# Performance work log

Measured on AMD Instinct MI355X. Metric: run time of the kernel, lower is better.

Reference implementation:

```python
import jax, jax.numpy as jnp
import numpy as np

ZETA = 1.03
GAMMA = -0.03


def setup_inputs() -> dict:
    key = jax.random.key(0)
    k1, k2, k3 = jax.random.split(key, 3)
    B, S, H, D = 2, 2048, 16, 128
    return {
        "query_states": jax.random.normal(k1, (B * S, H, D), dtype=jnp.float32),
        "key_states": jax.random.normal(k2, (B * S, H, D), dtype=jnp.float32),
        "value_states": jax.random.normal(k3, (B * S, H, D), dtype=jnp.float32),
        "batch_size": B,
        "q_length": S,
        "kv_length": S,
    }


def reference(query_states, key_states, value_states, batch_size, q_length, kv_length):
    H = query_states.shape[1]
    D = query_states.shape[2]
    # [B*S, H, D] -> [B, S, H, D]
    q = query_states.reshape(batch_size, q_length, H, D)
    k = key_states.reshape(batch_size, kv_length, H, D)
    v = value_states.reshape(batch_size, kv_length, H, D)
    # scores: [B, H, Q, K]
    scores = jnp.einsum("bqhd,bkhd->bhqk", q, k) / jnp.sqrt(jnp.float32(D)).astype(q.dtype)
    causal = jnp.triu(jnp.ones((q_length, kv_length), dtype=bool), k=1)  # True above diagonal
    scores = jnp.where(causal[None, None, :, :], -jnp.inf, scores)
    probs = jax.nn.softmax(scores, axis=-1)
    # clipped softmax (fp8 recipe): clip((zeta-gamma)*p + gamma, 0, 1)
    probs = jnp.clip((ZETA - GAMMA) * probs + GAMMA, 0.0, 1.0)
    out = jnp.einsum("bhqk,bkhd->bqhd", probs, v)
    return out.reshape(batch_size * q_length, H, D)
```

## Files before the change

### kernel.cpp

```cpp
#include <hip/hip_runtime.h>

typedef __attribute__((ext_vector_type(4))) float f32x4;
typedef __attribute__((ext_vector_type(8))) short bf16x8;
typedef __attribute__((ext_vector_type(4))) int   i32x4;
typedef __attribute__((ext_vector_type(2))) int   i32x2;

#define B_ 2
#define S_ 2048
#define H_ 16
#define D_ 128
#define RS_ (H_ * D_)
#define LOG2E 1.44269504088896340736f
#define ZG 1.06f
#define GM (-0.03f)
#define QSC (0.08838834764831845f * LOG2E)

__device__ __forceinline__ ushort f2bf(float x) {
    uint u = __builtin_bit_cast(uint, x);
    u += 0x7FFFu + ((u >> 16) & 1u);
    return (ushort)(u >> 16);
}

__device__ __forceinline__ void gld16(const void* g, void* l) {
    __builtin_amdgcn_global_load_lds(
        (const __attribute__((address_space(1))) unsigned int*)g,
        (__attribute__((address_space(3))) unsigned int*)l, 16, 0, 0);
}

__global__ __launch_bounds__(256)
void prep_kv(const float* __restrict__ Kg, const float* __restrict__ Vg,
             ushort* __restrict__ Kb, ushort* __restrict__ Vt)
{
    __shared__ ushort Vl[64 * 136];
    const int t = threadIdx.x;
    if (blockIdx.x < 512) {
        const int n  = blockIdx.x;
        const int bh = n >> 4;
        const int ch = n & 15;
        const int s  = ch * 128 + (t >> 1);
        const int d0 = (t & 1) * 64;
        const int b  = bh >> 4, h = bh & 15;
        const float* in = Kg + (((size_t)b * S_ + s) * H_ + h) * D_ + d0;
        ushort* out = Kb + ((size_t)bh * S_ + s) * D_ + d0;
#pragma unroll
        for (int j = 0; j < 4; ++j) {
            f32x4 x0 = *(const f32x4*)(in + j * 16);
            f32x4 x1 = *(const f32x4*)(in + j * 16 + 4);
            f32x4 x2 = *(const f32x4*)(in + j * 16 + 8);
            f32x4 x3 = *(const f32x4*)(in + j * 16 + 12);
            union { ushort u[16]; i32x4 v[2]; } p;
#pragma unroll
            for (int i = 0; i < 4; ++i) {
                p.u[i]      = f2bf(x0[i]);
                p.u[4 + i]  = f2bf(x1[i]);
                p.u[8 + i]  = f2bf(x2[i]);
                p.u[12 + i] = f2bf(x3[i]);
            }
            *(i32x4*)(out + j * 16)     = p.v[0];
            *(i32x4*)(out + j * 16 + 8) = p.v[1];
        }
    } else {
        const int n  = blockIdx.x - 512;
        const int bh = n >> 5;
        const int kt = n & 31;
        const int b  = bh >> 4, h = bh & 15;
#pragma unroll
        for (int it = 0; it < 2; ++it) {
            const int r  = it * 32 + (t >> 3);
            const int c0 = (t & 7) * 16;
            const int s  = kt * 64 + r;
            const float* in = Vg + (((size_t)b * S_ + s) * H_ + h) * D_ + c0;
            f32x4 x0 = *(const f32x4*)(in);
            f32x4 x1 = *(const f32x4*)(in + 4);
            f32x4 x2 = *(const f32x4*)(in + 8);
            f32x4 x3 = *(const f32x4*)(in + 12);
            union { ushort u[16]; i32x4 v[2]; } p;
#pragma unroll
            for (int i = 0; i < 4; ++i) {
                p.u[i]      = f2bf(x0[i]);
                p.u[4 + i]  = f2bf(x1[i]);
                p.u[8 + i]  = f2bf(x2[i]);
                p.u[12 + i] = f2bf(x3[i]);
            }
            *(i32x4*)(Vl + r * 136 + c0)     = p.v[0];
            *(i32x4*)(Vl + r * 136 + c0 + 8) = p.v[1];
        }
        __syncthreads();
        const int d  = t >> 1;
        const int kh = (t & 1) * 32;
        ushort* out = Vt + ((size_t)bh * 32 + kt) * 8192 + d * 64 + kh;
        uint wds[16];
#pragma unroll
        for (int i = 0; i < 16; ++i) {
            uint a = Vl[(kh + 2 * i) * 136 + d];
            uint c = Vl[(kh + 2 * i + 1) * 136 + d];
            wds[i] = a | (c << 16);
        }
#pragma unroll
        for (int j = 0; j < 4; ++j)
            *(i32x4*)(out + j * 8) = *(i32x4*)&wds[j * 4];
    }
}

__global__ __launch_bounds__(256, 3)
void attn_one(const float* __restrict__ Qg, const ushort* __restrict__ Kb,
              const ushort* __restrict__ Vt, float* __restrict__ Og)
{
    __shared__ char SHc[32768 + 4 * 2304];

    const int tid  = threadIdx.x;
    const int w    = tid >> 6;
    const int lane = tid & 63;
    const int g    = lane >> 4;
    const int l15  = lane & 15;
    char* const Kl = SHc;
    char* const Vl = SHc + 16384;
    char* const pB = SHc + 32768 + w * 2304;

    const int n  = blockIdx.x;
    const int qt = 31 - (n >> 5);
    const int bh = n & 31;
    const int b  = bh >> 4, h = bh & 15;

    const int q0  = qt * 64;
    const int qw0 = q0 + w * 16;
    const int qme = qw0 + l15;

    const float*  Qbh = Qg + ((size_t)b * S_ * H_ + h) * D_;
    const ushort* Kp  = Kb + (size_t)bh * S_ * D_;
    const ushort* Vp  = Vt + (size_t)bh * 32 * 8192;

    auto stageK2 = [&](int kt) {
#pragma unroll
        for (int i = 0; i < 8; ++i) {
            const int u = (w * 8 + i) * 64 + lane;
            const int r = u >> 4, cc = u & 15;
            const ushort* src = Kp + (size_t)(kt * 128 + r) * 128 + ((cc ^ (r & 15)) * 8);
            gld16(src, SHc + (w * 8 + i) * 1024);
        }
    };
    auto stageKV = [&](int kt) {
#pragma unroll
        for (int i = 0; i < 4; ++i) {
            const int u = (w * 4 + i) * 64 + lane;
            const int r = u >> 4, cc = u & 15;
            const ushort* src = Kp + (size_t)(kt * 64 + r) * 128 + ((cc ^ (r & 15)) * 8);
            gld16(src, Kl + (w * 4 + i) * 1024);
        }
        const ushort* tile = Vp + (size_t)kt * 8192;
#pragma unroll
        for (int i = 0; i < 4; ++i) {
            const int u = (w * 4 + i) * 64 + lane;
            const int r = u >> 3, cc = u & 7;
            const ushort* src = tile + r * 64 + ((cc ^ (r & 7)) * 8);
            gld16(src, Vl + (w * 4 + i) * 1024);
        }
    };

    stageK2(0);

    bf16x8 qf[4];
    {
        const float* qptr = Qbh + (size_t)qme * RS_;
#pragma unroll
        for (int db = 0; db < 4; ++db) {
            const float* p = qptr + db * 32 + g * 8;
            f32x4 a = *(const f32x4*)p;
            f32x4 d = *(const f32x4*)(p + 4);
#pragma unroll
            for (int i = 0; i < 4; ++i) {
                qf[db][i]     = (short)f2bf(a[i] * QSC);
                qf[db][i + 4] = (short)f2bf(d[i] * QSC);
            }
        }
    }
    asm volatile("s_waitcnt vmcnt(0)" ::: "memory");
    __syncthreads();

    float acc = 0.f;
    const int kt1 = (q0 + 191) >> 7;
#pragma unroll 1
    for (int kt = 0; kt < kt1; ++kt) {
        const ushort* K2 = (const ushort*)SHc;
        f32x4 s[8];
#pragma unroll
        for (int cc = 0; cc < 8; ++cc) s[cc] = (f32x4){0.f, 0.f, 0.f, 0.f};
        __builtin_amdgcn_s_setprio(1);
#pragma unroll
        for (int db = 0; db < 4; ++db) {
            const int usw = ((db * 4 + g) ^ l15) * 8;
#pragma unroll
            for (int cc = 0; cc < 8; ++cc) {
                bf16x8 kf = *(const bf16x8*)(K2 + (cc * 16 + l15) * 128 + usw);
                s[cc] = __builtin_amdgcn_mfma_f32_16x16x32_bf16(kf, qf[db], s[cc], 0, 0, 0);
            }
        }
        __builtin_amdgcn_s_setprio(0);
        if (kt == kt1 - 1) {
#pragma unroll
            for (int cc = 0; cc < 8; ++cc) {
                const int key0 = kt * 128 + cc * 16 + g * 4;
#pragma unroll
                for (int r = 0; r < 4; ++r) {
                    const float e = exp2f(s[cc][r]);
                    acc += (key0 + r <= qme) ? e : 0.f;
                }
            }
        } else {
#pragma unroll
            for (int cc = 0; cc < 8; ++cc)
#pragma unroll
                for (int r = 0; r < 4; ++r)
                    acc += exp2f(s[cc][r]);
        }
        __syncthreads();
        if (kt + 1 < kt1) {
            stageK2(kt + 1);
            asm volatile("s_waitcnt vmcnt(0)" ::: "memory");
        }
        __syncthreads();
    }

    stageKV(0);

    float c1;
    {
        float t = acc;
        t += __shfl_xor(t, 16);
        t += __shfl_xor(t, 32);
        c1 = ZG / t;
    }
    const float thr = log2f(-GM / c1);
    asm volatile("s_waitcnt vmcnt(0)" ::: "memory");
    __syncthreads();

    f32x4 o[8];
#pragma unroll
    for (int db = 0; db < 8; ++db) o[db] = (f32x4){0.f, 0.f, 0.f, 0.f};

    const int kt2 = qt + 1;
#pragma unroll 1
    for (int kt = 0; kt < kt2; ++kt) {
        f32x4 s[4];
#pragma unroll
        for (int cb = 0; cb < 4; ++cb) s[cb] = (f32x4){0.f, 0.f, 0.f, 0.f};
        __builtin_amdgcn_s_setprio(1);
#pragma unroll
        for (int db = 0; db < 4; ++db) {
            const int usw = ((db * 4 + g) ^ l15) * 8;
#pragma unroll
            for (int cb = 0; cb < 4; ++cb) {
                bf16x8 kf = *(const bf16x8*)((const ushort*)Kl + (cb * 16 + l15) * 128 + usw);
                s[cb] = __builtin_amdgcn_mfma_f32_16x16x32_bf16(kf, qf[db], s[cb], 0, 0, 0);
            }
        }
        __builtin_amdgcn_s_setprio(0);

        float smax = fmaxf(fmaxf(fmaxf(s[0][0], s[0][1]), fmaxf(s[0][2], s[0][3])),
                           fmaxf(fmaxf(s[1][0], s[1][1]), fmaxf(s[1][2], s[1][3])));
        smax = fmaxf(smax,
               fmaxf(fmaxf(fmaxf(s[2][0], s[2][1]), fmaxf(s[2][2], s[2][3])),
                     fmaxf(fmaxf(s[3][0], s[3][1]), fmaxf(s[3][2], s[3][3]))));

        if (__any(smax > thr)) {
            const bool diag = (kt == kt2 - 1);
#pragma unroll
            for (int cb = 0; cb < 4; ++cb) {
                const int key0 = kt * 64 + cb * 16 + g * 4;
                float p[4];
#pragma unroll
                for (int r = 0; r < 4; ++r) {
                    float e = exp2f(s[cb][r]);
                    if (diag) e = (key0 + r <= qme) ? e : 0.f;
                    p[r] = fminf(fmaxf(c1 * e + GM, 0.f), 1.f);
                }
                uint r01, r23;
                asm("v_cvt_pk_bf16_f32 %0, %1, %2" : "=v"(r01) : "v"(p[0]), "v"(p[1]));
                asm("v_cvt_pk_bf16_f32 %0, %1, %2" : "=v"(r23) : "v"(p[2]), "v"(p[3]));
                i32x2 pv2 = {(int)r01, (int)r23};
                *(i32x2*)(pB + l15 * 144 + cb * 32 + g * 8) = pv2;
            }
            asm volatile("s_waitcnt lgkmcnt(0)" ::: "memory");
            f32x4 onew[8];
            __builtin_amdgcn_s_setprio(1);
#pragma unroll
            for (int ks = 0; ks < 2; ++ks) {
                bf16x8 pf = *(const bf16x8*)(pB + l15 * 144 + ks * 64 + g * 16);
#pragma unroll
                for (int db = 0; db < 8; ++db) {
                    const int d = db * 16 + l15;
                    bf16x8 vf = *(const bf16x8*)(Vl + d * 128 +
                                                 (((ks * 4 + g) ^ (d & 7)) * 16));
                    f32x4& dst = (ks == 0) ? onew[db] : o[db];
                    const f32x4 src = (ks == 0) ? o[db] : onew[db];
                    dst = __builtin_amdgcn_mfma_f32_16x16x32_bf16(pf, vf, src, 0, 0, 0);
                }
            }
            __builtin_amdgcn_s_setprio(0);
        }
        __syncthreads();
        if (kt + 1 < kt2) {
            stageKV(kt + 1);
            asm volatile("s_waitcnt vmcnt(0)" ::: "memory");
        }
        __syncthreads();
    }

    const size_t orow0 = ((size_t)(b * S_ + qw0) * H_ + h) * D_;
#pragma unroll
    for (int db = 0; db < 8; ++db) {
#pragma unroll
        for (int r = 0; r < 4; ++r) {
            const int qr = g * 4 + r;
            Og[orow0 + (size_t)qr * RS_ + db * 16 + l15] = o[db][r];
        }
    }
}

__global__ __launch_bounds__(256, 2)
void attn_fwd(const float* __restrict__ Qg, const float* __restrict__ Kg,
              const float* __restrict__ Vg, float* __restrict__ Og)
{
    __shared__ ushort Kl[32 * 128];
    __shared__ ushort Vt[128 * 40];
    __shared__ ushort Pl[4][16 * 40];

    const int tid  = threadIdx.x;
    const int w    = tid >> 6;
    const int lane = tid & 63;
    const int g    = lane >> 4;
    const int l15  = lane & 15;

    const int q0 = blockIdx.x * 64;
    const int bh = blockIdx.y;
    const int b  = bh >> 4;
    const int h  = bh & (H_ - 1);

    const size_t bh_off = ((size_t)b * S_ * H_ + h) * D_;
    const float* Qp = Qg + bh_off;
    const float* Kp = Kg + bh_off;
    const float* Vp = Vg + bh_off;

    const int qw0 = q0 + w * 16;
    const int wave_last_q = qw0 + 15;
    bf16x8 qf[4];
    {
        const float* qptr = Qp + (size_t)(qw0 + l15) * RS_;
        const float sc = 0.08838834764831845f;
#pragma unroll
        for (int db = 0; db < 4; ++db) {
            const float* p = qptr + db * 32 + g * 8;
            f32x4 a = *(const f32x4*)p;
            f32x4 c = *(const f32x4*)(p + 4);
#pragma unroll
            for (int i = 0; i < 4; ++i) {
                qf[db][i]     = (short)f2bf(a[i] * sc);
                qf[db][i + 4] = (short)f2bf(c[i] * sc);
            }
        }
    }

    char* const klB = (char*)Kl;
    char* const vtB = (char*)Vt;
    const int kr  = tid >> 3;
    const int kcu = (tid & 7) * 2;
    const int vk  = (tid >> 5) * 4;
    const int vd  = (tid & 31) * 4;

    auto stageK = [&](int kt0) {
        const float* p = Kp + (size_t)(kt0 + kr) * RS_ + kcu * 8;
        f32x4 x0 = *(const f32x4*)(p);
        f32x4 x1 = *(const f32x4*)(p + 4);
        f32x4 x2 = *(const f32x4*)(p + 8);
        f32x4 x3 = *(const f32x4*)(p + 12);
        union { ushort u[8]; i32x4 v; } a, c;
#pragma unroll
        for (int i = 0; i < 4; ++i) {
            a.u[i]     = f2bf(x0[i]);
            a.u[i + 4] = f2bf(x1[i]);
            c.u[i]     = f2bf(x2[i]);
            c.u[i + 4] = f2bf(x3[i]);
        }
        const int sw = kr & 7;
        *(i32x4*)(klB + kr * 256 + ((kcu ^ sw) * 16))       = a.v;
        *(i32x4*)(klB + kr * 256 + (((kcu + 1) ^ sw) * 16)) = c.v;
    };

    auto stageV = [&](int kt0) {
        ushort t[4][4];
#pragma unroll
        for (int i = 0; i < 4; ++i) {
            const f32x4 x = *(const f32x4*)(Vp + (size_t)(kt0 + vk + i) * RS_ + vd);
#pragma unroll
            for (int j = 0; j < 4; ++j) t[i][j] = f2bf(x[j]);
        }
#pragma unroll
        for (int j = 0; j < 4; ++j) {
            union { ushort u[4]; i32x2 v; } pk;
#pragma unroll
            for (int i = 0; i < 4; ++i) pk.u[i] = t[i][j];
            *(i32x2*)(vtB + (size_t)(vd + j) * 80 + vk * 2) = pk.v;
        }
    };

    auto qkTile = [&](f32x4& s0, f32x4& s1) {
        s0 = (f32x4){0.f, 0.f, 0.f, 0.f};
        s1 = (f32x4){0.f, 0.f, 0.f, 0.f};
        const int swz = l15 & 7;
#pragma unroll
        for (int db = 0; db < 4; ++db) {
            const int unit = db * 4 + g;
            bf16x8 k0 = *(const bf16x8*)(klB + l15 * 256 + ((unit ^ swz) * 16));
            bf16x8 k1 = *(const bf16x8*)(klB + (l15 + 16) * 256 + ((unit ^ swz) * 16));
            s0 = __builtin_amdgcn_mfma_f32_16x16x32_bf16(qf[db], k0, s0, 0, 0, 0);
            s1 = __builtin_amdgcn_mfma_f32_16x16x32_bf16(qf[db], k1, s1, 0, 0, 0);
        }
    };

    const int ktiles = (q0 + 64) / 32;

    float m[4] = {-1e30f, -1e30f, -1e30f, -1e30f};
    float l[4] = {0.f, 0.f, 0.f, 0.f};

    for (int kt = 0; kt < ktiles; ++kt) {
        const int kt0 = kt * 32;
        __syncthreads();
        stageK(kt0);
        __syncthreads();
        if (kt0 > wave_last_q) continue;
        f32x4 s0, s1;
        qkTile(s0, s1);
#pragma unroll
        for (int r = 0; r < 4; ++r) {
            const int qq = qw0 + g * 4 + r;
            const int ke = kt0 + l15;
            float v0 = (ke <= qq)      ? s0[r] : -1e30f;
            float v1 = (ke + 16 <= qq) ? s1[r] : -1e30f;
            float tmax = fmaxf(v0, v1);
            tmax = fmaxf(tmax, __shfl_xor(tmax, 1));
            tmax = fmaxf(tmax, __shfl_xor(tmax, 2));
            tmax = fmaxf(tmax, __shfl_xor(tmax, 4));
            tmax = fmaxf(tmax, __shfl_xor(tmax, 8));
            const float mn = fmaxf(m[r], tmax);
            float es = exp2f((v0 - mn) * LOG2E) + exp2f((v1 - mn) * LOG2E);
            es += __shfl_xor(es, 1);
            es += __shfl_xor(es, 2);
            es += __shfl_xor(es, 4);
            es += __shfl_xor(es, 8);
            l[r] = l[r] * exp2f((m[r] - mn) * LOG2E) + es;
            m[r] = mn;
        }
    }

    float c1[4];
#pragma unroll
    for (int r = 0; r < 4; ++r) c1[r] = ZG / l[r];

    f32x4 o[8];
#pragma unroll
    for (int db = 0; db < 8; ++db) o[db] = (f32x4){0.f, 0.f, 0.f, 0.f};

    char* const pB = (char*)(Pl[w]);

    for (int kt = 0; kt < ktiles; ++kt) {
        const int kt0 = kt * 32;
        __syncthreads();
        stageK(kt0);
        stageV(kt0);
        __syncthreads();
        if (kt0 > wave_last_q) continue;
        f32x4 s0, s1;
        qkTile(s0, s1);
#pragma unroll
        for (int r = 0; r < 4; ++r) {
            const int qq = qw0 + g * 4 + r;
            const int ke = kt0 + l15;
            float v0 = (ke <= qq)      ? s0[r] : -1e30f;
            float v1 = (ke + 16 <= qq) ? s1[r] : -1e30f;
            float p0 = c1[r] * exp2f((v0 - m[r]) * LOG2E) + GM;
            float p1 = c1[r] * exp2f((v1 - m[r]) * LOG2E) + GM;
            p0 = fminf(fmaxf(p0, 0.f), 1.f);
            p1 = fminf(fmaxf(p1, 0.f), 1.f);
            const int qr = g * 4 + r;
            *(ushort*)(pB + qr * 80 + l15 * 2)        = f2bf(p0);
            *(ushort*)(pB + qr * 80 + (l15 + 16) * 2) = f2bf(p1);
        }
        asm volatile("s_waitcnt lgkmcnt(0)" ::: "memory");
        bf16x8 pf = *(const bf16x8*)(pB + l15 * 80 + g * 16);
#pragma unroll
        for (int db = 0; db < 8; ++db) {
            bf16x8 vf = *(const bf16x8*)(vtB + (size_t)(db * 16 + l15) * 80 + g * 16);
            o[db] = __builtin_amdgcn_mfma_f32_16x16x32_bf16(pf, vf, o[db], 0, 0, 0);
        }
    }

    const size_t orow0 = ((size_t)(b * S_ + qw0) * H_ + h) * D_;
#pragma unroll
    for (int db = 0; db < 8; ++db) {
#pragma unroll
        for (int r = 0; r < 4; ++r) {
            const int qr = g * 4 + r;
            Og[orow0 + (size_t)qr * RS_ + db * 16 + l15] = o[db][r];
        }
    }
}

extern "C" void kernel_launch(void* const* d_in, const int* in_sizes, int n_in,
                              void* d_out, int out_size, void* d_ws, size_t ws_size,
                              hipStream_t stream)
{
    const float* Q = (const float*)d_in[0];
    const float* K = (const float*)d_in[1];
    const float* V = (const float*)d_in[2];
    (void)in_sizes; (void)n_in; (void)out_size;

    if (ws_size >= (size_t)33554432) {
        ushort* Kb = (ushort*)d_ws;
        ushort* Vt = (ushort*)d_ws + 8388608;
        prep_kv<<<dim3(1536), dim3(256), 0, stream>>>(K, V, Kb, Vt);
        attn_one<<<dim3(1024), dim3(256), 0, stream>>>(Q, Kb, Vt, (float*)d_out);
    } else {
        attn_fwd<<<dim3(S_ / 64, B_ * H_), dim3(256), 0, stream>>>(Q, K, V, (float*)d_out);
    }
}
```

Baseline: 91.41 us.

## Skip KV tiles whose max score cannot exceed clipped-softmax threshold

```diff
diff --git a/kernel.cpp b/kernel.cpp
--- a/kernel.cpp
+++ b/kernel.cpp
@@ -106,16 +106,18 @@
 void attn_one(const float* __restrict__ Qg, const ushort* __restrict__ Kb,
               const ushort* __restrict__ Vt, float* __restrict__ Og)
 {
-    __shared__ char SHc[32768 + 4 * 2304];
+    __shared__ char SHc[32768 + 4 * 2304 + 4096 + 16];
 
     const int tid  = threadIdx.x;
     const int w    = tid >> 6;
     const int lane = tid & 63;
     const int g    = lane >> 4;
     const int l15  = lane & 15;
-    char* const Kl = SHc;
-    char* const Vl = SHc + 16384;
-    char* const pB = SHc + 32768 + w * 2304;
+    char*  const Kl    = SHc;
+    char*  const Vl    = SHc + 16384;
+    char*  const pB    = SHc + 32768 + w * 2304;
+    float* const SmaxL = (float*)(SHc + 41984);
+    uint*  const Flags = (uint*)(SHc + 46080);
 
     const int n  = blockIdx.x;
     const int qt = 31 - (n >> 5);
@@ -196,23 +198,31 @@
             }
         }
         __builtin_amdgcn_s_setprio(0);
+        float sm = -1e30f;
         if (kt == kt1 - 1) {
 #pragma unroll
             for (int cc = 0; cc < 8; ++cc) {
                 const int key0 = kt * 128 + cc * 16 + g * 4;
 #pragma unroll
                 for (int r = 0; r < 4; ++r) {
+                    const bool ok = (key0 + r <= qme);
                     const float e = exp2f(s[cc][r]);
-                    acc += (key0 + r <= qme) ? e : 0.f;
+                    acc += ok ? e : 0.f;
+                    sm = fmaxf(sm, ok ? s[cc][r] : -1e30f);
                 }
             }
         } else {
 #pragma unroll
             for (int cc = 0; cc < 8; ++cc)
 #pragma unroll
-                for (int r = 0; r < 4; ++r)
+                for (int r = 0; r < 4; ++r) {
                     acc += exp2f(s[cc][r]);
-        }
+                    sm = fmaxf(sm, s[cc][r]);
+                }
+        }
+        sm = fmaxf(sm, __shfl_xor(sm, 16));
+        sm = fmaxf(sm, __shfl_xor(sm, 32));
+        if (lane < 16) SmaxL[(w * 16 + kt) * 16 + l15] = sm;
         __syncthreads();
         if (kt + 1 < kt1) {
             stageK2(kt + 1);
@@ -220,8 +230,6 @@
         }
         __syncthreads();
     }
-
-    stageKV(0);
 
     float c1;
     {
@@ -231,6 +239,21 @@
         c1 = ZG / t;
     }
     const float thr = log2f(-GM / c1);
+
+    uint mymask = 0;
+#pragma unroll 1
+    for (int st = 0; st < kt1; ++st) {
+        const float sm = SmaxL[(w * 16 + st) * 16 + l15];
+        if (__any(sm > thr)) mymask |= (1u << st);
+    }
+    if (lane == 0) Flags[w] = mymask;
+    __syncthreads();
+    const uint blockmask = Flags[0] | Flags[1] | Flags[2] | Flags[3];
+
+    const int kt2 = qt + 1;
+    int kt = 0;
+    while (kt < kt2 && !((blockmask >> (kt >> 1)) & 1u)) ++kt;
+    if (kt < kt2) stageKV(kt);
     asm volatile("s_waitcnt vmcnt(0)" ::: "memory");
     __syncthreads();
 
@@ -238,9 +261,8 @@
 #pragma unroll
     for (int db = 0; db < 8; ++db) o[db] = (f32x4){0.f, 0.f, 0.f, 0.f};
 
-    const int kt2 = qt + 1;
 #pragma unroll 1
-    for (int kt = 0; kt < kt2; ++kt) {
+    while (kt < kt2) {
         f32x4 s[4];
 #pragma unroll
         for (int cb = 0; cb < 4; ++cb) s[cb] = (f32x4){0.f, 0.f, 0.f, 0.f};
@@ -298,12 +320,16 @@
             }
             __builtin_amdgcn_s_setprio(0);
         }
-        __syncthreads();
-        if (kt + 1 < kt2) {
-            stageKV(kt + 1);
+
+        int nkt = kt + 1;
+        while (nkt < kt2 && !((blockmask >> (nkt >> 1)) & 1u)) ++nkt;
+        __syncthreads();
+        if (nkt < kt2) {
+            stageKV(nkt);
             asm volatile("s_waitcnt vmcnt(0)" ::: "memory");
         }
         __syncthreads();
+        kt = nkt;
     }
 
     const size_t orow0 = ((size_t)(b * S_ + qw0) * H_ + h) * D_;
```

Result: faster. 83.45 us (median of 2 runs) (-8.7%).
